# Kernel optimization log

Hardware: AMD Instinct MI355X
Metric: run time of the kernel (lower is better)

## Reference

```python
import jax, jax.numpy as jnp
import numpy as np

B, S, H, T = 32, 512, 256, 48
START_IDX, STOP_IDX = 46, 47
NEG = -10000.0


def setup_inputs() -> dict:
    key = jax.random.key(0)
    k1, k2, k3, k4, k5 = jax.random.split(key, 5)
    lstm_features = jax.random.normal(k1, (B, S, H), dtype=jnp.float32)
    emission_w = jax.random.normal(k2, (H, T), dtype=jnp.float32) * 0.02
    emission_b = jnp.zeros((T,), dtype=jnp.float32)
    transitions = jax.random.normal(k3, (T, T), dtype=jnp.float32)
    transitions = transitions.at[:, START_IDX].set(NEG).at[STOP_IDX, :].set(NEG)
    lengths = jax.random.randint(k4, (B,), S // 2, S + 1, dtype=jnp.int32)
    tags = jax.random.randint(k5, (B, S), 0, START_IDX, dtype=jnp.int32)
    return {
        'lstm_features': lstm_features,
        'emission_w': emission_w,
        'emission_b': emission_b,
        'transitions': transitions,
        'lengths': lengths,
        'tags': tags,
    }


def _crf_scores(lstm_features, emission_w, emission_b, transitions):
    # emission: [B,S,T] at the 'to' tag; crf[b,s,i,j] = emission[b,s,j] + transitions[i,j]
    em = jnp.einsum('bsh,ht->bst', lstm_features, emission_w) + emission_b
    return em[:, :, None, :] + transitions[None, None, :, :]


def _forward_alg(crf_scores, transitions, lengths):
    # alpha[b,j] = log-sum-exp over paths ending at tag j
    alpha0 = jnp.full((B, T), NEG, dtype=crf_scores.dtype).at[:, START_IDX].set(0.0)

    def step(alpha, xs):
        crf_t, t = xs  # crf_t: [B,T,T]
        tag_var = crf_t + alpha[:, :, None]  # add score of 'from' tag
        new_alpha = jax.scipy.special.logsumexp(tag_var, axis=1)  # reduce over 'from'
        alpha = jnp.where((t < lengths)[:, None], new_alpha, alpha)
        return alpha, None

    xs = (jnp.swapaxes(crf_scores, 0, 1), jnp.arange(S, dtype=lengths.dtype))
    alpha, _ = jax.lax.scan(step, alpha0, xs)
    terminal = alpha + transitions[:, STOP_IDX][None, :]
    return jax.scipy.special.logsumexp(terminal, axis=1)  # [B]


def _gold_score(crf_scores, transitions, tags, lengths):
    # from_tags[t] = START for t=0 else tags[t-1]; to_tags[t] = tags[t]
    start_col = jnp.full((B, 1), START_IDX, dtype=tags.dtype)
    from_tags = jnp.concatenate([start_col, tags[:, :-1]], axis=1)  # [B,S]
    b_idx = jnp.arange(B)[:, None]
    s_idx = jnp.arange(S)[None, :]
    sel = crf_scores[b_idx, s_idx, from_tags, tags]  # [B,S]
    mask = (s_idx < lengths[:, None]).astype(sel.dtype)
    last_tag = jnp.take_along_axis(tags, (lengths - 1)[:, None], axis=1)[:, 0]
    return jnp.sum(sel * mask, axis=1) + transitions[last_tag, STOP_IDX]  # [B]


def reference(lstm_features, emission_w, emission_b, transitions, lengths, tags):
    crf_scores = _crf_scores(lstm_features, emission_w, emission_b, transitions)
    all_paths = _forward_alg(crf_scores, transitions, lengths)
    gold = _gold_score(crf_scores, transitions, tags, lengths)
    return all_paths - gold  # per-example NLL, shape [B]
```

## Files before the change

kernel.cpp:

```cpp
#include <hip/hip_runtime.h>
#include <math.h>

#define BB 32
#define SS 512
#define HH 256
#define TT 48
#define START_IDX 46
#define STOP_IDX 47

typedef __attribute__((ext_vector_type(8))) short short8;
typedef __attribute__((ext_vector_type(4))) float floatx4;

__device__ __forceinline__ float rfl(float x) {
    return __int_as_float(__builtin_amdgcn_readfirstlane(__float_as_int(x)));
}
__device__ __forceinline__ unsigned short bf16_rne(float x) {
    const unsigned int u = __float_as_uint(x);
    return (unsigned short)((u + 0x7fffu + ((u >> 16) & 1u)) >> 16);
}
__device__ __forceinline__ float bf2f(unsigned short h) {
    return __uint_as_float(((unsigned int)h) << 16);
}

__global__ __launch_bounds__(256) void emission_kernel(
    const float* __restrict__ f, const float* __restrict__ w,
    const float* __restrict__ bias, unsigned short* __restrict__ exem)
{
    __shared__ __align__(16) unsigned short wb[HH * 50];
    __shared__ __align__(16) uint4 fragbuf[24 * 64];
    __shared__ float biaslds[TT];

    const int tid = threadIdx.x;
    for (int idx = tid; idx < HH * TT; idx += 256) {
        const int r = idx / TT;
        const int c = idx - r * TT;
        wb[r * 50 + c] = bf16_rne(w[idx]);
    }
    if (tid < TT) biaslds[tid] = bias[tid];
    __syncthreads();

    for (int idx = tid; idx < 24 * 64; idx += 256) {
        const int fb = idx >> 6;
        const int l  = idx & 63;
        const int kt = fb / 3;
        const int nt = fb - kt * 3;
        const int kbase = kt * 32 + (l >> 4) * 8;
        const int col   = nt * 16 + (l & 15);
        unsigned int p[4];
#pragma unroll
        for (int h = 0; h < 4; ++h) {
            const unsigned int lo = wb[(kbase + 2 * h)     * 50 + col];
            const unsigned int hi = wb[(kbase + 2 * h + 1) * 50 + col];
            p[h] = lo | (hi << 16);
        }
        fragbuf[idx] = make_uint4(p[0], p[1], p[2], p[3]);
    }
    __syncthreads();

    const int lane = tid & 63;
    const int wv   = tid >> 6;

    short8 Bf[24];
#pragma unroll
    for (int fb = 0; fb < 24; ++fb)
        Bf[fb] = __builtin_bit_cast(short8, fragbuf[fb * 64 + lane]);

    const int row = blockIdx.x * 64 + wv * 16 + (lane & 15);
    const float* frow = f + (size_t)row * HH + (lane >> 4) * 8;

    floatx4 acc0 = {0.f, 0.f, 0.f, 0.f};
    floatx4 acc1 = {0.f, 0.f, 0.f, 0.f};
    floatx4 acc2 = {0.f, 0.f, 0.f, 0.f};
#pragma unroll
    for (int kt = 0; kt < 8; ++kt) {
        const float4 v0 = *(const float4*)(frow + kt * 32);
        const float4 v1 = *(const float4*)(frow + kt * 32 + 4);
        const unsigned int a0 = bf16_rne(v0.x) | ((unsigned int)bf16_rne(v0.y) << 16);
        const unsigned int a1 = bf16_rne(v0.z) | ((unsigned int)bf16_rne(v0.w) << 16);
        const unsigned int a2 = bf16_rne(v1.x) | ((unsigned int)bf16_rne(v1.y) << 16);
        const unsigned int a3 = bf16_rne(v1.z) | ((unsigned int)bf16_rne(v1.w) << 16);
        const short8 Af = __builtin_bit_cast(short8, make_uint4(a0, a1, a2, a3));
        acc0 = __builtin_amdgcn_mfma_f32_16x16x32_bf16(Af, Bf[kt * 3 + 0], acc0, 0, 0, 0);
        acc1 = __builtin_amdgcn_mfma_f32_16x16x32_bf16(Af, Bf[kt * 3 + 1], acc1, 0, 0, 0);
        acc2 = __builtin_amdgcn_mfma_f32_16x16x32_bf16(Af, Bf[kt * 3 + 2], acc2, 0, 0, 0);
    }

    const int outrow0 = blockIdx.x * 64 + wv * 16 + (lane >> 4) * 4;
    const int n = lane & 15;
#pragma unroll
    for (int r = 0; r < 4; ++r) {
        unsigned short* e = exem + (size_t)(outrow0 + r) * TT;
        e[ 0 + n] = bf16_rne(__expf(acc0[r] + biaslds[ 0 + n]));
        e[16 + n] = bf16_rne(__expf(acc1[r] + biaslds[16 + n]));
        e[32 + n] = bf16_rne(__expf(acc2[r] + biaslds[32 + n]));
    }
}

__global__ __launch_bounds__(64) void chunk_kernel(
    const unsigned short* __restrict__ exem,
    const float* __restrict__ trans,
    const int*   __restrict__ lengths,
    unsigned short* __restrict__ Qs,
    float* __restrict__ Ls)
{
    __shared__ __align__(16) unsigned short abuf[49 * 56];
    __shared__ __align__(16) unsigned short ebuf[16 * TT];

    const int bc = blockIdx.x;
    const int b = bc >> 5, c = bc & 31;
    const int len = lengths[b];
    int nsteps = (len - 1) - (c << 4);
    if (nsteps <= 0) return;
    if (nsteps > 16) nsteps = 16;

    const int j = threadIdx.x, g = j >> 4, cl = j & 15;

    {
        const unsigned int* src = (const unsigned int*)(exem + ((size_t)b * SS + (c << 4)) * TT);
        unsigned int* dst = (unsigned int*)ebuf;
#pragma unroll
        for (int i = 0; i < 6; ++i) dst[j + i * 64] = src[j + i * 64];
    }

    uint4 Bf[2][3];
#pragma unroll
    for (int kc = 0; kc < 2; ++kc)
#pragma unroll
        for (int nt = 0; nt < 3; ++nt) {
            unsigned int p[4];
#pragma unroll
            for (int h = 0; h < 4; ++h) {
                const int k = kc * 32 + g * 8 + 2 * h;
                const int n = nt * 16 + cl;
                const float lo = (k     < TT) ? __expf(trans[k * TT + n])       : 0.f;
                const float hi = (k + 1 < TT) ? __expf(trans[(k + 1) * TT + n]) : 0.f;
                p[h] = (unsigned int)bf16_rne(lo) | ((unsigned int)bf16_rne(hi) << 16);
            }
            Bf[kc][nt] = make_uint4(p[0], p[1], p[2], p[3]);
        }

    floatx4 acc[3][3];
#pragma unroll
    for (int mt = 0; mt < 3; ++mt)
#pragma unroll
        for (int nt = 0; nt < 3; ++nt)
#pragma unroll
            for (int r = 0; r < 4; ++r)
                acc[mt][nt][r] = (mt == nt && (4 * g + r) == cl) ? 1.f : 0.f;

    float sigprev = 1.f, L = 0.f;
    float ev[3];
#pragma unroll
    for (int nt = 0; nt < 3; ++nt) ev[nt] = bf2f(ebuf[nt * 16 + cl]);

    for (int s = 0; s < nsteps; ++s) {
        float invsig = 1.f;
        if (s) { L += __logf(sigprev); invsig = __builtin_amdgcn_rcpf(sigprev); }
        float fs[3];
#pragma unroll
        for (int nt = 0; nt < 3; ++nt) fs[nt] = ev[nt] * invsig;

#pragma unroll
        for (int mt = 0; mt < 3; ++mt)
#pragma unroll
            for (int nt = 0; nt < 3; ++nt)
#pragma unroll
                for (int r = 0; r < 4; ++r)
                    abuf[(mt * 16 + 4 * g + r) * 56 + nt * 16 + cl] =
                        bf16_rne(acc[mt][nt][r] * fs[nt]);

        if (s + 1 < nsteps) {
#pragma unroll
            for (int nt = 0; nt < 3; ++nt)
                ev[nt] = bf2f(ebuf[(s + 1) * TT + nt * 16 + cl]);
        }

        uint4 Af[3][2];
#pragma unroll
        for (int mt = 0; mt < 3; ++mt) {
            Af[mt][0] = *(const uint4*)&abuf[(mt * 16 + cl) * 56 + g * 8];
            uint4 a1  = *(const uint4*)&abuf[(mt * 16 + cl) * 56 + 32 + g * 8];
            if (g >= 2) a1 = make_uint4(0, 0, 0, 0);
            Af[mt][1] = a1;
        }

        const floatx4 z = {0.f, 0.f, 0.f, 0.f};
#pragma unroll
        for (int mt = 0; mt < 3; ++mt)
#pragma unroll
            for (int nt = 0; nt < 3; ++nt) {
                floatx4 d = __builtin_amdgcn_mfma_f32_16x16x32_bf16(
                    __builtin_bit_cast(short8, Af[mt][0]),
                    __builtin_bit_cast(short8, Bf[0][nt]), z, 0, 0, 0);
                d = __builtin_amdgcn_mfma_f32_16x16x32_bf16(
                    __builtin_bit_cast(short8, Af[mt][1]),
                    __builtin_bit_cast(short8, Bf[1][nt]), d, 0, 0, 0);
                acc[mt][nt] = d;
            }
        sigprev = rfl(acc[0][0][0]);
    }

    unsigned short* qb = Qs + (size_t)bc * (TT * 64);
#pragma unroll
    for (int mt = 0; mt < 3; ++mt)
#pragma unroll
        for (int nt = 0; nt < 3; ++nt) {
            const int col = nt * 16 + cl, row0 = mt * 16 + 4 * g;
            const unsigned int lo = (unsigned int)bf16_rne(acc[mt][nt][0])
                                  | ((unsigned int)bf16_rne(acc[mt][nt][1]) << 16);
            const unsigned int hi = (unsigned int)bf16_rne(acc[mt][nt][2])
                                  | ((unsigned int)bf16_rne(acc[mt][nt][3]) << 16);
            *(uint2*)&qb[col * 64 + row0] = make_uint2(lo, hi);
        }
    if (j == 0) Ls[bc] = L;
}

__global__ __launch_bounds__(64) void finalize_kernel(
    const unsigned short* __restrict__ exem,
    const float* __restrict__ trans,
    const int*   __restrict__ lengths,
    const int*   __restrict__ tags,
    const unsigned short* __restrict__ Qs,
    const float* __restrict__ Ls,
    float* __restrict__ out)
{
    __shared__ float tlds[TT * TT];
    __shared__ __align__(16) unsigned short vlds[64];

    const int j = threadIdx.x, b = blockIdx.x, g = j >> 4, cl = j & 15;

    for (int idx = j; idx < TT * TT; idx += 64) tlds[idx] = trans[idx];
    __builtin_amdgcn_wave_barrier();

    const int len = lengths[b];

    float gold = 0.f;
    for (int s = j; s < len; s += 64) {
        const int tag  = tags[b * SS + s];
        const int from = (s == 0) ? START_IDX : tags[b * SS + s - 1];
        gold += __logf(bf2f(exem[((size_t)b * SS + s) * TT + tag])) + tlds[from * TT + tag];
    }
    gold += __shfl_xor(gold, 32); gold += __shfl_xor(gold, 16); gold += __shfl_xor(gold, 8);
    gold += __shfl_xor(gold, 4);  gold += __shfl_xor(gold, 2);  gold += __shfl_xor(gold, 1);

    const float vj = (j < TT) ? __expf(tlds[START_IDX * TT + j]) : 0.f;
    vlds[j] = bf16_rne(vj);

    const int nc = (len - 1 + 15) >> 4;
    const unsigned short* qbase = Qs + (size_t)(b * 32) * (TT * 64);

    float L = 0.f, inv = 1.f;
    floatx4 accn[3];

    uint4 pB0[3], pB1[3];
#pragma unroll
    for (int nt = 0; nt < 3; ++nt) {
        pB0[nt] = *(const uint4*)&qbase[(size_t)0 * TT * 64 + (nt * 16 + cl) * 64 + g * 8];
        pB1[nt] = *(const uint4*)&qbase[(size_t)0 * TT * 64 + (nt * 16 + cl) * 64 + 32 + g * 8];
    }

    for (int cc = 0; cc < nc; ++cc) {
        uint4 B0[3], B1[3];
#pragma unroll
        for (int nt = 0; nt < 3; ++nt) { B0[nt] = pB0[nt]; B1[nt] = pB1[nt]; }

        const int cn = (cc + 1 < nc) ? cc + 1 : cc;
#pragma unroll
        for (int nt = 0; nt < 3; ++nt) {
            pB0[nt] = *(const uint4*)&qbase[(size_t)cn * TT * 64 + (nt * 16 + cl) * 64 + g * 8];
            pB1[nt] = *(const uint4*)&qbase[(size_t)cn * TT * 64 + (nt * 16 + cl) * 64 + 32 + g * 8];
        }

#pragma unroll
        for (int nt = 0; nt < 3; ++nt)
            if (g >= 2) B1[nt] = make_uint4(0, 0, 0, 0);

        const uint4 A0 = *(const uint4*)&vlds[g * 8];
        const uint4 A1 = *(const uint4*)&vlds[32 + g * 8];

        const floatx4 z = {0.f, 0.f, 0.f, 0.f};
#pragma unroll
        for (int nt = 0; nt < 3; ++nt) {
            floatx4 d = __builtin_amdgcn_mfma_f32_16x16x32_bf16(
                __builtin_bit_cast(short8, A0), __builtin_bit_cast(short8, B0[nt]), z, 0, 0, 0);
            d = __builtin_amdgcn_mfma_f32_16x16x32_bf16(
                __builtin_bit_cast(short8, A1), __builtin_bit_cast(short8, B1[nt]), d, 0, 0, 0);
            accn[nt] = d;
        }

        const float sig = rfl(accn[0][0]);
        inv = __builtin_amdgcn_rcpf(sig);
        L += __logf(sig) + Ls[b * 32 + cc];

        if (j < 16) {
#pragma unroll
            for (int nt = 0; nt < 3; ++nt)
                vlds[nt * 16 + j] = bf16_rne(accn[nt][0] * inv);
        }
    }

    float term = 0.f;
    if (j < 16) {
        const size_t erow = ((size_t)b * SS + (len - 1)) * TT;
#pragma unroll
        for (int nt = 0; nt < 3; ++nt) {
            const int col = nt * 16 + j;
            term += accn[nt][0] * inv * bf2f(exem[erow + col])
                    * __expf(tlds[col * TT + STOP_IDX]);
        }
    }
    term += __shfl_xor(term, 32); term += __shfl_xor(term, 16); term += __shfl_xor(term, 8);
    term += __shfl_xor(term, 4);  term += __shfl_xor(term, 2);  term += __shfl_xor(term, 1);

    if (j == 0) {
        const float all_paths = __logf(term) + L;
        const int last = tags[b * SS + len - 1];
        out[b] = all_paths - (gold + tlds[last * TT + STOP_IDX]);
    }
}

extern "C" void kernel_launch(void* const* d_in, const int* in_sizes, int n_in,
                              void* d_out, int out_size, void* d_ws, size_t ws_size,
                              hipStream_t stream) {
    const float* f       = (const float*)d_in[0];
    const float* w       = (const float*)d_in[1];
    const float* bias    = (const float*)d_in[2];
    const float* trans   = (const float*)d_in[3];
    const int*   lengths = (const int*)d_in[4];
    const int*   tags    = (const int*)d_in[5];
    float*       out     = (float*)d_out;

    unsigned short* exem = (unsigned short*)d_ws;
    unsigned short* Qs   = exem + (size_t)BB * SS * TT;
    float*          Lsc  = (float*)(Qs + (size_t)BB * 32 * TT * 64);

    emission_kernel<<<(BB * SS) / 64, 256, 0, stream>>>(f, w, bias, exem);
    chunk_kernel<<<BB * 32, 64, 0, stream>>>(exem, trans, lengths, Qs, Lsc);
    finalize_kernel<<<BB, 64, 0, stream>>>(exem, trans, lengths, tags, Qs, Lsc, out);
}
```

Before: 121.4 us.

## Split chunk matrix chain across three waves and precompute exp-transition fragments once

The chunk kernel now runs three waves per chunk, each owning one 16-row block of the 48x48 transfer matrix. Each step therefore issues 6 MFMAs per wave instead of 18 in a single wave. Renormalization changes from every step to a single per-row-block rescale at step 8, with the per-block log scales folded into the finalize kernel. The exp(transitions) bf16 MFMA fragments are built once by block 0 of the emission kernel instead of by every chunk block. The emission kernel also stages the feature rows through LDS with coalesced float4 loads. The trade-offs are more LDS per block, extra bookkeeping in finalize, and a possible loss of precision from less frequent rescaling.

```diff
diff --git a/kernel.cpp b/kernel.cpp
--- a/kernel.cpp
+++ b/kernel.cpp
@@ -14,9 +14,9 @@
 __device__ __forceinline__ float rfl(float x) {
     return __int_as_float(__builtin_amdgcn_readfirstlane(__float_as_int(x)));
 }
-__device__ __forceinline__ unsigned short bf16_rne(float x) {
+__device__ __forceinline__ unsigned int bf16_rne(float x) {
     const unsigned int u = __float_as_uint(x);
-    return (unsigned short)((u + 0x7fffu + ((u >> 16) & 1u)) >> 16);
+    return (u + 0x7fffu + ((u >> 16) & 1u)) >> 16;
 }
 __device__ __forceinline__ float bf2f(unsigned short h) {
     return __uint_as_float(((unsigned int)h) << 16);
@@ -24,17 +24,40 @@
 
 __global__ __launch_bounds__(256) void emission_kernel(
     const float* __restrict__ f, const float* __restrict__ w,
-    const float* __restrict__ bias, unsigned short* __restrict__ exem)
+    const float* __restrict__ bias, const float* __restrict__ trans,
+    unsigned short* __restrict__ exem, uint4* __restrict__ Ebuf)
 {
-    __shared__ __align__(16) unsigned short wb[HH * 50];
-    __shared__ __align__(16) uint4 fragbuf[24 * 64];
+    __shared__ __align__(16) char smem[50176];
     __shared__ float biaslds[TT];
+    unsigned short* wb = (unsigned short*)smem;
+    uint4* fragbuf = (uint4*)(smem + 25600);
+    float* fl = (float*)smem;
 
     const int tid = threadIdx.x;
+
+    if (blockIdx.x == 0 && tid < 64) {
+        const int g = tid >> 4, cl = tid & 15;
+#pragma unroll
+        for (int kc = 0; kc < 2; ++kc)
+#pragma unroll
+            for (int nt = 0; nt < 3; ++nt) {
+                unsigned int p[4];
+#pragma unroll
+                for (int h2 = 0; h2 < 4; ++h2) {
+                    const int k = kc * 32 + g * 8 + 2 * h2;
+                    const int n = nt * 16 + cl;
+                    const float lo = (k     < TT) ? __expf(trans[k * TT + n])       : 0.f;
+                    const float hi = (k + 1 < TT) ? __expf(trans[(k + 1) * TT + n]) : 0.f;
+                    p[h2] = bf16_rne(lo) | (bf16_rne(hi) << 16);
+                }
+                Ebuf[(kc * 3 + nt) * 64 + tid] = make_uint4(p[0], p[1], p[2], p[3]);
+            }
+    }
+
     for (int idx = tid; idx < HH * TT; idx += 256) {
         const int r = idx / TT;
         const int c = idx - r * TT;
-        wb[r * 50 + c] = bf16_rne(w[idx]);
+        wb[r * 50 + c] = (unsigned short)bf16_rne(w[idx]);
     }
     if (tid < TT) biaslds[tid] = bias[tid];
     __syncthreads();
@@ -48,171 +71,156 @@
         const int col   = nt * 16 + (l & 15);
         unsigned int p[4];
 #pragma unroll
-        for (int h = 0; h < 4; ++h) {
-            const unsigned int lo = wb[(kbase + 2 * h)     * 50 + col];
-            const unsigned int hi = wb[(kbase + 2 * h + 1) * 50 + col];
-            p[h] = lo | (hi << 16);
+        for (int h2 = 0; h2 < 4; ++h2) {
+            const unsigned int lo = wb[(kbase + 2 * h2)     * 50 + col];
+            const unsigned int hi = wb[(kbase + 2 * h2 + 1) * 50 + col];
+            p[h2] = lo | (hi << 16);
         }
         fragbuf[idx] = make_uint4(p[0], p[1], p[2], p[3]);
     }
     __syncthreads();
 
-    const int lane = tid & 63;
-    const int wv   = tid >> 6;
+    const int lane = tid & 63, wv = tid >> 6, g = lane >> 4, cl = lane & 15;
 
     short8 Bf[24];
 #pragma unroll
     for (int fb = 0; fb < 24; ++fb)
         Bf[fb] = __builtin_bit_cast(short8, fragbuf[fb * 64 + lane]);
-
-    const int row = blockIdx.x * 64 + wv * 16 + (lane & 15);
-    const float* frow = f + (size_t)row * HH + (lane >> 4) * 8;
-
-    floatx4 acc0 = {0.f, 0.f, 0.f, 0.f};
-    floatx4 acc1 = {0.f, 0.f, 0.f, 0.f};
-    floatx4 acc2 = {0.f, 0.f, 0.f, 0.f};
-#pragma unroll
-    for (int kt = 0; kt < 8; ++kt) {
-        const float4 v0 = *(const float4*)(frow + kt * 32);
-        const float4 v1 = *(const float4*)(frow + kt * 32 + 4);
-        const unsigned int a0 = bf16_rne(v0.x) | ((unsigned int)bf16_rne(v0.y) << 16);
-        const unsigned int a1 = bf16_rne(v0.z) | ((unsigned int)bf16_rne(v0.w) << 16);
-        const unsigned int a2 = bf16_rne(v1.x) | ((unsigned int)bf16_rne(v1.y) << 16);
-        const unsigned int a3 = bf16_rne(v1.z) | ((unsigned int)bf16_rne(v1.w) << 16);
-        const short8 Af = __builtin_bit_cast(short8, make_uint4(a0, a1, a2, a3));
-        acc0 = __builtin_amdgcn_mfma_f32_16x16x32_bf16(Af, Bf[kt * 3 + 0], acc0, 0, 0, 0);
-        acc1 = __builtin_amdgcn_mfma_f32_16x16x32_bf16(Af, Bf[kt * 3 + 1], acc1, 0, 0, 0);
-        acc2 = __builtin_amdgcn_mfma_f32_16x16x32_bf16(Af, Bf[kt * 3 + 2], acc2, 0, 0, 0);
-    }
-
-    const int outrow0 = blockIdx.x * 64 + wv * 16 + (lane >> 4) * 4;
-    const int n = lane & 15;
+    __syncthreads();
+
+    const int row0 = blockIdx.x * 64;
+    floatx4 acc0 = {0.f,0.f,0.f,0.f}, acc1 = {0.f,0.f,0.f,0.f}, acc2 = {0.f,0.f,0.f,0.f};
+
+    const int lr = wv * 16 + cl;
+#pragma unroll
+    for (int h = 0; h < 2; ++h) {
+#pragma unroll
+        for (int it = 0; it < 8; ++it) {
+            const int idx = tid + it * 256;
+            const int r = idx >> 5, k4 = idx & 31;
+            const float4 v = ((const float4*)f)[(size_t)(row0 + r) * 64 + h * 32 + k4];
+            *(float4*)&fl[r * 132 + k4 * 4] = v;
+        }
+        __syncthreads();
+#pragma unroll
+        for (int kt = 0; kt < 4; ++kt) {
+            const float4 v0 = *(const float4*)&fl[lr * 132 + kt * 32 + g * 8];
+            const float4 v1 = *(const float4*)&fl[lr * 132 + kt * 32 + g * 8 + 4];
+            const unsigned int a0 = bf16_rne(v0.x) | (bf16_rne(v0.y) << 16);
+            const unsigned int a1 = bf16_rne(v0.z) | (bf16_rne(v0.w) << 16);
+            const unsigned int a2 = bf16_rne(v1.x) | (bf16_rne(v1.y) << 16);
+            const unsigned int a3 = bf16_rne(v1.z) | (bf16_rne(v1.w) << 16);
+            const short8 Af = __builtin_bit_cast(short8, make_uint4(a0, a1, a2, a3));
+            const int kg = h * 4 + kt;
+            acc0 = __builtin_amdgcn_mfma_f32_16x16x32_bf16(Af, Bf[kg * 3 + 0], acc0, 0, 0, 0);
+            acc1 = __builtin_amdgcn_mfma_f32_16x16x32_bf16(Af, Bf[kg * 3 + 1], acc1, 0, 0, 0);
+            acc2 = __builtin_amdgcn_mfma_f32_16x16x32_bf16(Af, Bf[kg * 3 + 2], acc2, 0, 0, 0);
+        }
+        __syncthreads();
+    }
+
+    const int outrow0 = row0 + wv * 16 + g * 4;
+    const int n = cl;
 #pragma unroll
     for (int r = 0; r < 4; ++r) {
         unsigned short* e = exem + (size_t)(outrow0 + r) * TT;
-        e[ 0 + n] = bf16_rne(__expf(acc0[r] + biaslds[ 0 + n]));
-        e[16 + n] = bf16_rne(__expf(acc1[r] + biaslds[16 + n]));
-        e[32 + n] = bf16_rne(__expf(acc2[r] + biaslds[32 + n]));
-    }
-}
-
-__global__ __launch_bounds__(64) void chunk_kernel(
+        e[ 0 + n] = (unsigned short)bf16_rne(__expf(acc0[r] + biaslds[ 0 + n]));
+        e[16 + n] = (unsigned short)bf16_rne(__expf(acc1[r] + biaslds[16 + n]));
+        e[32 + n] = (unsigned short)bf16_rne(__expf(acc2[r] + biaslds[32 + n]));
+    }
+}
+
+__global__ __launch_bounds__(192) void chunk_kernel(
     const unsigned short* __restrict__ exem,
-    const float* __restrict__ trans,
+    const uint4* __restrict__ Ebuf,
     const int*   __restrict__ lengths,
     unsigned short* __restrict__ Qs,
-    float* __restrict__ Ls)
+    float* __restrict__ Ls3)
 {
-    __shared__ __align__(16) unsigned short abuf[49 * 56];
-    __shared__ __align__(16) unsigned short ebuf[16 * TT];
-
-    const int bc = blockIdx.x;
-    const int b = bc >> 5, c = bc & 31;
+    __shared__ __align__(8)  unsigned short ebuf[16 * TT];
+    __shared__ __align__(16) unsigned short abuf[3][17 * 56];
+
+    const int bc = blockIdx.x, b = bc >> 5, c = bc & 31;
     const int len = lengths[b];
     int nsteps = (len - 1) - (c << 4);
     if (nsteps <= 0) return;
     if (nsteps > 16) nsteps = 16;
 
-    const int j = threadIdx.x, g = j >> 4, cl = j & 15;
+    const int tid = threadIdx.x;
+    const int rb = tid >> 6, l = tid & 63, g = l >> 4, cl = l & 15;
 
     {
         const unsigned int* src = (const unsigned int*)(exem + ((size_t)b * SS + (c << 4)) * TT);
         unsigned int* dst = (unsigned int*)ebuf;
-#pragma unroll
-        for (int i = 0; i < 6; ++i) dst[j + i * 64] = src[j + i * 64];
+        dst[tid] = src[tid];
+        dst[tid + 192] = src[tid + 192];
     }
 
     uint4 Bf[2][3];
 #pragma unroll
     for (int kc = 0; kc < 2; ++kc)
 #pragma unroll
-        for (int nt = 0; nt < 3; ++nt) {
-            unsigned int p[4];
-#pragma unroll
-            for (int h = 0; h < 4; ++h) {
-                const int k = kc * 32 + g * 8 + 2 * h;
-                const int n = nt * 16 + cl;
-                const float lo = (k     < TT) ? __expf(trans[k * TT + n])       : 0.f;
-                const float hi = (k + 1 < TT) ? __expf(trans[(k + 1) * TT + n]) : 0.f;
-                p[h] = (unsigned int)bf16_rne(lo) | ((unsigned int)bf16_rne(hi) << 16);
-            }
-            Bf[kc][nt] = make_uint4(p[0], p[1], p[2], p[3]);
-        }
-
-    floatx4 acc[3][3];
-#pragma unroll
-    for (int mt = 0; mt < 3; ++mt)
-#pragma unroll
         for (int nt = 0; nt < 3; ++nt)
-#pragma unroll
-            for (int r = 0; r < 4; ++r)
-                acc[mt][nt][r] = (mt == nt && (4 * g + r) == cl) ? 1.f : 0.f;
-
-    float sigprev = 1.f, L = 0.f;
+            Bf[kc][nt] = Ebuf[(kc * 3 + nt) * 64 + l];
+
+    __syncthreads();
+
+    floatx4 acc[3];
+#pragma unroll
+    for (int nt = 0; nt < 3; ++nt)
+#pragma unroll
+        for (int r = 0; r < 4; ++r)
+            acc[nt][r] = (16 * rb + 4 * g + r == nt * 16 + cl) ? 1.f : 0.f;
+
     float ev[3];
 #pragma unroll
     for (int nt = 0; nt < 3; ++nt) ev[nt] = bf2f(ebuf[nt * 16 + cl]);
 
+    float Lrb = 0.f;
+    unsigned short* aw = abuf[rb];
+
     for (int s = 0; s < nsteps; ++s) {
-        float invsig = 1.f;
-        if (s) { L += __logf(sigprev); invsig = __builtin_amdgcn_rcpf(sigprev); }
-        float fs[3];
-#pragma unroll
-        for (int nt = 0; nt < 3; ++nt) fs[nt] = ev[nt] * invsig;
-
-#pragma unroll
-        for (int mt = 0; mt < 3; ++mt)
-#pragma unroll
-            for (int nt = 0; nt < 3; ++nt)
-#pragma unroll
-                for (int r = 0; r < 4; ++r)
-                    abuf[(mt * 16 + 4 * g + r) * 56 + nt * 16 + cl] =
-                        bf16_rne(acc[mt][nt][r] * fs[nt]);
-
+        float scale = 1.f;
+        if (s == 8) {
+            const float sig = rfl(acc[0][0]);
+            Lrb = __logf(sig);
+            scale = __builtin_amdgcn_rcpf(sig);
+        }
+        const float f0 = ev[0] * scale, f1 = ev[1] * scale, f2 = ev[2] * scale;
+#pragma unroll
+        for (int r = 0; r < 4; ++r) {
+            const int rw = (4 * g + r) * 56;
+            aw[rw +      cl] = (unsigned short)bf16_rne(acc[0][r] * f0);
+            aw[rw + 16 + cl] = (unsigned short)bf16_rne(acc[1][r] * f1);
+            aw[rw + 32 + cl] = (unsigned short)bf16_rne(acc[2][r] * f2);
+        }
         if (s + 1 < nsteps) {
 #pragma unroll
             for (int nt = 0; nt < 3; ++nt)
                 ev[nt] = bf2f(ebuf[(s + 1) * TT + nt * 16 + cl]);
         }
-
-        uint4 Af[3][2];
-#pragma unroll
-        for (int mt = 0; mt < 3; ++mt) {
-            Af[mt][0] = *(const uint4*)&abuf[(mt * 16 + cl) * 56 + g * 8];
-            uint4 a1  = *(const uint4*)&abuf[(mt * 16 + cl) * 56 + 32 + g * 8];
-            if (g >= 2) a1 = make_uint4(0, 0, 0, 0);
-            Af[mt][1] = a1;
-        }
-
+        uint4 a0 = *(const uint4*)&aw[cl * 56 + g * 8];
+        uint4 a1 = *(const uint4*)&aw[cl * 56 + 32 + g * 8];
+        if (g >= 2) a1 = make_uint4(0, 0, 0, 0);
         const floatx4 z = {0.f, 0.f, 0.f, 0.f};
 #pragma unroll
-        for (int mt = 0; mt < 3; ++mt)
-#pragma unroll
-            for (int nt = 0; nt < 3; ++nt) {
-                floatx4 d = __builtin_amdgcn_mfma_f32_16x16x32_bf16(
-                    __builtin_bit_cast(short8, Af[mt][0]),
-                    __builtin_bit_cast(short8, Bf[0][nt]), z, 0, 0, 0);
-                d = __builtin_amdgcn_mfma_f32_16x16x32_bf16(
-                    __builtin_bit_cast(short8, Af[mt][1]),
-                    __builtin_bit_cast(short8, Bf[1][nt]), d, 0, 0, 0);
-                acc[mt][nt] = d;
-            }
-        sigprev = rfl(acc[0][0][0]);
+        for (int nt = 0; nt < 3; ++nt) {
+            floatx4 d = __builtin_amdgcn_mfma_f32_16x16x32_bf16(
+                __builtin_bit_cast(short8, a0), __builtin_bit_cast(short8, Bf[0][nt]), z, 0, 0, 0);
+            d = __builtin_amdgcn_mfma_f32_16x16x32_bf16(
+                __builtin_bit_cast(short8, a1), __builtin_bit_cast(short8, Bf[1][nt]), d, 0, 0, 0);
+            acc[nt] = d;
+        }
     }
 
     unsigned short* qb = Qs + (size_t)bc * (TT * 64);
 #pragma unroll
-    for (int mt = 0; mt < 3; ++mt)
-#pragma unroll
-        for (int nt = 0; nt < 3; ++nt) {
-            const int col = nt * 16 + cl, row0 = mt * 16 + 4 * g;
-            const unsigned int lo = (unsigned int)bf16_rne(acc[mt][nt][0])
-                                  | ((unsigned int)bf16_rne(acc[mt][nt][1]) << 16);
-            const unsigned int hi = (unsigned int)bf16_rne(acc[mt][nt][2])
-                                  | ((unsigned int)bf16_rne(acc[mt][nt][3]) << 16);
-            *(uint2*)&qb[col * 64 + row0] = make_uint2(lo, hi);
-        }
-    if (j == 0) Ls[bc] = L;
+    for (int nt = 0; nt < 3; ++nt) {
+        const unsigned int lo = bf16_rne(acc[nt][0]) | (bf16_rne(acc[nt][1]) << 16);
+        const unsigned int hi = bf16_rne(acc[nt][2]) | (bf16_rne(acc[nt][3]) << 16);
+        *(uint2*)&qb[(nt * 16 + cl) * 64 + 16 * rb + 4 * g] = make_uint2(lo, hi);
+    }
+    if (l == 0) Ls3[bc * 3 + rb] = Lrb;
 }
 
 __global__ __launch_bounds__(64) void finalize_kernel(
@@ -221,18 +229,21 @@
     const int*   __restrict__ lengths,
     const int*   __restrict__ tags,
     const unsigned short* __restrict__ Qs,
-    const float* __restrict__ Ls,
+    const float* __restrict__ Ls3,
     float* __restrict__ out)
 {
     __shared__ float tlds[TT * TT];
     __shared__ __align__(16) unsigned short vlds[64];
+    __shared__ float Lsl[96];
 
     const int j = threadIdx.x, b = blockIdx.x, g = j >> 4, cl = j & 15;
 
     for (int idx = j; idx < TT * TT; idx += 64) tlds[idx] = trans[idx];
+
+    const int len = lengths[b];
+    const int nc = (len - 1 + 15) >> 4;
+    for (int i = j; i < nc * 3; i += 64) Lsl[i] = Ls3[b * 96 + i];
     __builtin_amdgcn_wave_barrier();
-
-    const int len = lengths[b];
 
     float gold = 0.f;
     for (int s = j; s < len; s += 64) {
@@ -243,20 +254,21 @@
     gold += __shfl_xor(gold, 32); gold += __shfl_xor(gold, 16); gold += __shfl_xor(gold, 8);
     gold += __shfl_xor(gold, 4);  gold += __shfl_xor(gold, 2);  gold += __shfl_xor(gold, 1);
 
-    const float vj = (j < TT) ? __expf(tlds[START_IDX * TT + j]) : 0.f;
-    vlds[j] = bf16_rne(vj);
-
-    const int nc = (len - 1 + 15) >> 4;
+    const float R0 = Lsl[0];
+    float vj = 0.f;
+    if (j < TT) vj = __expf(tlds[START_IDX * TT + j]) * __expf(Lsl[j >> 4] - R0);
+    vlds[j] = (unsigned short)bf16_rne(vj);
+    float L = R0;
+
     const unsigned short* qbase = Qs + (size_t)(b * 32) * (TT * 64);
-
-    float L = 0.f, inv = 1.f;
     floatx4 accn[3];
+    float inv = 1.f;
 
     uint4 pB0[3], pB1[3];
 #pragma unroll
     for (int nt = 0; nt < 3; ++nt) {
-        pB0[nt] = *(const uint4*)&qbase[(size_t)0 * TT * 64 + (nt * 16 + cl) * 64 + g * 8];
-        pB1[nt] = *(const uint4*)&qbase[(size_t)0 * TT * 64 + (nt * 16 + cl) * 64 + 32 + g * 8];
+        pB0[nt] = *(const uint4*)&qbase[(nt * 16 + cl) * 64 + g * 8];
+        pB1[nt] = *(const uint4*)&qbase[(nt * 16 + cl) * 64 + 32 + g * 8];
     }
 
     for (int cc = 0; cc < nc; ++cc) {
@@ -270,7 +282,6 @@
             pB0[nt] = *(const uint4*)&qbase[(size_t)cn * TT * 64 + (nt * 16 + cl) * 64 + g * 8];
             pB1[nt] = *(const uint4*)&qbase[(size_t)cn * TT * 64 + (nt * 16 + cl) * 64 + 32 + g * 8];
         }
-
 #pragma unroll
         for (int nt = 0; nt < 3; ++nt)
             if (g >= 2) B1[nt] = make_uint4(0, 0, 0, 0);
@@ -290,12 +301,20 @@
 
         const float sig = rfl(accn[0][0]);
         inv = __builtin_amdgcn_rcpf(sig);
-        L += __logf(sig) + Ls[b * 32 + cc];
-
-        if (j < 16) {
-#pragma unroll
-            for (int nt = 0; nt < 3; ++nt)
-                vlds[nt * 16 + j] = bf16_rne(accn[nt][0] * inv);
+
+        if (cc + 1 < nc) {
+            const float Rn = Lsl[(cc + 1) * 3];
+            const float fa0 = __expf(Lsl[(cc + 1) * 3 + 0] - Rn);
+            const float fa1 = __expf(Lsl[(cc + 1) * 3 + 1] - Rn);
+            const float fa2 = __expf(Lsl[(cc + 1) * 3 + 2] - Rn);
+            L += __logf(sig) + Rn;
+            if (j < 16) {
+                vlds[ 0 + j] = (unsigned short)bf16_rne(accn[0][0] * inv * fa0);
+                vlds[16 + j] = (unsigned short)bf16_rne(accn[1][0] * inv * fa1);
+                vlds[32 + j] = (unsigned short)bf16_rne(accn[2][0] * inv * fa2);
+            }
+        } else {
+            L += __logf(sig);
         }
     }
 
@@ -330,11 +349,13 @@
     const int*   tags    = (const int*)d_in[5];
     float*       out     = (float*)d_out;
 
-    unsigned short* exem = (unsigned short*)d_ws;
-    unsigned short* Qs   = exem + (size_t)BB * SS * TT;
-    float*          Lsc  = (float*)(Qs + (size_t)BB * 32 * TT * 64);
-
-    emission_kernel<<<(BB * SS) / 64, 256, 0, stream>>>(f, w, bias, exem);
-    chunk_kernel<<<BB * 32, 64, 0, stream>>>(exem, trans, lengths, Qs, Lsc);
+    char* ws = (char*)d_ws;
+    unsigned short* exem = (unsigned short*)ws;
+    unsigned short* Qs   = (unsigned short*)(ws + 1572864);
+    float*          Lsc  = (float*)(ws + 7864320);
+    uint4*          Ebuf = (uint4*)(ws + 7876608);
+
+    emission_kernel<<<(BB * SS) / 64, 256, 0, stream>>>(f, w, bias, trans, exem, Ebuf);
+    chunk_kernel<<<BB * 32, 192, 0, stream>>>(exem, Ebuf, lengths, Qs, Lsc);
     finalize_kernel<<<BB, 64, 0, stream>>>(exem, trans, lengths, tags, Qs, Lsc, out);
 }
```

New measurement: 116.7 us, median of 2. -3.9%, faster.
